# Optimization experiments

Hardware: AMD Instinct MI355X
Metric: run time of the kernel (lower is better)

The kernel has to match this reference:

```python
import jax, jax.numpy as jnp
import numpy as np

D = 256  # MCB sketch/output dimension


def count_sketch(x, h, s, d=D):
    # x: [B,H,W,C] channel-last; h: [C] int hash indices in [0,d); s: [C] +/-1 signs
    xs = x * s
    return jnp.zeros(x.shape[:-1] + (d,), x.dtype).at[..., h].add(xs)


def mcb(x, y, h1, s1, h2, s2, d=D):
    # Compact bilinear pooling per spatial location. x,y: [B,C,H,W] -> [B,d,H,W]
    xt = jnp.moveaxis(x, 1, -1)
    yt = jnp.moveaxis(y, 1, -1)
    fx = jnp.fft.rfft(count_sketch(xt, h1, s1, d), axis=-1)
    fy = jnp.fft.rfft(count_sketch(yt, h2, s2, d), axis=-1)
    out = jnp.fft.irfft(fx * fy, n=d, axis=-1)  # circular convolution of the two sketches
    return jnp.moveaxis(out, -1, 1)


def setup_inputs() -> dict:
    key = jax.random.key(0)
    ks = jax.random.split(key, 10)
    B, C, H, W, ATTR = 64, 256, 28, 28, 300
    entity_feature = jax.random.normal(ks[0], (B, C, H, W), jnp.float32)
    attr_one_hot = jax.random.uniform(ks[1], (B, ATTR), jnp.float32)
    W_emb = jax.random.normal(ks[2], (C, ATTR), jnp.float32) * 0.05
    b_emb = jax.random.normal(ks[3], (C,), jnp.float32) * 0.01
    h1 = jax.random.randint(ks[4], (C,), 0, D, jnp.int32)
    h2 = jax.random.randint(ks[5], (C,), 0, D, jnp.int32)
    s1 = jnp.where(jax.random.bernoulli(ks[6], 0.5, (C,)), 1.0, -1.0).astype(jnp.float32)
    s2 = jnp.where(jax.random.bernoulli(ks[7], 0.5, (C,)), 1.0, -1.0).astype(jnp.float32)
    conv1_w = jax.random.normal(ks[8], (32, C), jnp.float32) * 0.05
    conv2_w = jax.random.normal(ks[9], (1, 32), jnp.float32) * 0.05
    return {"entity_feature": entity_feature, "attr_one_hot": attr_one_hot,
            "W_emb": W_emb, "b_emb": b_emb, "h1": h1, "s1": s1, "h2": h2, "s2": s2,
            "conv1_w": conv1_w, "conv2_w": conv2_w}


def reference(entity_feature, attr_one_hot, W_emb, b_emb, h1, s1, h2, s2, conv1_w, conv2_w):
    # textual embedding: Linear(attr_num -> 256)
    emb = attr_one_hot @ W_emb.T + b_emb                      # [B,256]
    attr = jnp.broadcast_to(emb[:, :, None, None], entity_feature.shape)  # expand_as
    mcb_feat = mcb(attr, entity_feature, h1, s1, h2, s2)      # [B,256,H,W]
    hidden = jax.nn.relu(jnp.einsum('bchw,oc->bohw', mcb_feat, conv1_w))  # conv1x1 256->32
    attr_map = jax.nn.sigmoid(jnp.einsum('bchw,oc->bohw', hidden, conv2_w))  # conv1x1 32->1
    attr_feature = attr_map * entity_feature
    return attr_map, attr_feature
```

## Files before the change

### kernel.cpp

```cpp
#include <hip/hip_runtime.h>
#include <math.h>

#define BATCH 64
#define CC    256
#define ATTRN 300
#define DD    256
#define HW    784
#define HW4   196
#define O1    32
#define TF4   49


__global__ __launch_bounds__(512) void k2_fused(
    const float* __restrict__ attr_one_hot,
    const float* __restrict__ W_emb,
    const float* __restrict__ b_emb,
    const int*   __restrict__ h1,
    const float* __restrict__ s1,
    const float* __restrict__ conv1_w,
    float* __restrict__ corrT)
{
    const int b = blockIdx.x, og = blockIdx.y;
    const int tid = threadIdx.x;
    const int t = tid & 255, kh = tid >> 8;
    const int o0 = og * 8;

    __shared__ float s_attr[ATTRN];
    __shared__ float s_sx[DD];
    __shared__ float s_w1[8][DD];
    __shared__ float s_part[8][DD];

    if (kh == 0) {
        s_sx[t] = 0.f;
        if (t < 75) {
            float4 a = *(const float4*)(attr_one_hot + b * ATTRN + 4 * t);
            *(float4*)&s_attr[4 * t] = a;
        }
    } else {
#pragma unroll
        for (int j = 0; j < 8; ++j) s_w1[j][t] = conv1_w[(o0 + j) * CC + t];
    }
    __syncthreads();

    if (kh == 0) {
        float acc = b_emb[t];
        const float* wr = W_emb + (size_t)t * ATTRN;
#pragma unroll 5
        for (int v = 0; v < 75; ++v) {
            float4 w = *(const float4*)(wr + 4 * v);
            float4 a = *(const float4*)(&s_attr[4 * v]);
            acc += w.x * a.x + w.y * a.y + w.z * a.z + w.w * a.w;
        }
        atomicAdd(&s_sx[h1[t]], s1[t] * acc);
    }
    __syncthreads();

    float acc[8] = {0.f,0.f,0.f,0.f,0.f,0.f,0.f,0.f};
    const int kbase = kh << 7;
    for (int k4 = 0; k4 < 32; ++k4) {
        const int k = kbase + 4 * k4;
        float x0 = s_sx[(k     - t) & 255];
        float x1 = s_sx[(k + 1 - t) & 255];
        float x2 = s_sx[(k + 2 - t) & 255];
        float x3 = s_sx[(k + 3 - t) & 255];
#pragma unroll
        for (int oo = 0; oo < 8; ++oo) {
            float4 w = *(const float4*)&s_w1[oo][k];
            acc[oo] += w.x * x0 + w.y * x1 + w.z * x2 + w.w * x3;
        }
    }
    if (kh == 1) {
#pragma unroll
        for (int oo = 0; oo < 8; ++oo) s_part[oo][t] = acc[oo];
    }
    __syncthreads();
    if (kh == 0) {
        float4 r0, r1;
        r0.x = acc[0] + s_part[0][t]; r0.y = acc[1] + s_part[1][t];
        r0.z = acc[2] + s_part[2][t]; r0.w = acc[3] + s_part[3][t];
        r1.x = acc[4] + s_part[4][t]; r1.y = acc[5] + s_part[5][t];
        r1.z = acc[6] + s_part[6][t]; r1.w = acc[7] + s_part[7][t];
        float4* dst = (float4*)(corrT + ((size_t)b * DD + t) * O1 + o0);
        dst[0] = r0; dst[1] = r1;
    }
}

#define FMA4(A, S, E) { (A).x += (S)*(E).x; (A).y += (S)*(E).y; (A).z += (S)*(E).z; (A).w += (S)*(E).w; }

__global__ __launch_bounds__(1024, 4) void k3_main(
    const float* __restrict__ ent,
    const float* __restrict__ corrT,
    const int*   __restrict__ h2,
    const float* __restrict__ s2,
    const float* __restrict__ conv2_w,
    float* __restrict__ out_map,
    float* __restrict__ out_feat)
{
    const int b = blockIdx.x, tile = blockIdx.y;
    const int tid  = threadIdx.x;
    const int wv   = tid >> 6, lane = tid & 63;
    const int ci   = wv >> 2;
    const int oi   = wv & 3;

    union SMem {
        float  Pl[CC][36];
        float4 red[4][TF4][9];
    };
    __shared__ SMem sm;
    __shared__ float4 s_amap4[TF4];
    __shared__ float  s_c2[O1];

    {
        const int c = tid >> 2, qp = tid & 3;
        const int hc = h2[c];
        const float sc = s2[c];
        const float4* src = (const float4*)(corrT + ((size_t)b * DD + hc) * O1);
        float4 x0 = src[2 * qp], x1 = src[2 * qp + 1];
        x0.x *= sc; x0.y *= sc; x0.z *= sc; x0.w *= sc;
        x1.x *= sc; x1.y *= sc; x1.z *= sc; x1.w *= sc;
        *(float4*)&sm.Pl[c][8 * qp]     = x0;
        *(float4*)&sm.Pl[c][8 * qp + 4] = x1;
        if (tid < O1) s_c2[tid] = conv2_w[tid];
    }
    __syncthreads();

    const bool act = lane < TF4;
    const int f4i = tile * TF4 + (act ? lane : TF4 - 1);
    const float4* ent4 = (const float4*)ent;
    const int c0 = ci * 64;

    float4 acc[8];
#pragma unroll
    for (int o = 0; o < 8; ++o) acc[o] = make_float4(0.f, 0.f, 0.f, 0.f);

    const float4* eptr = ent4 + (size_t)(b * CC + c0) * HW4 + f4i;
#pragma unroll 4
    for (int cc = 0; cc < 64; ++cc) {
        const int c = c0 + cc;
        float4 e4 = eptr[(size_t)cc * HW4];
        float4 pa = *(const float4*)&sm.Pl[c][8 * oi];
        float4 pb = *(const float4*)&sm.Pl[c][8 * oi + 4];
        FMA4(acc[0], pa.x, e4); FMA4(acc[1], pa.y, e4);
        FMA4(acc[2], pa.z, e4); FMA4(acc[3], pa.w, e4);
        FMA4(acc[4], pb.x, e4); FMA4(acc[5], pb.y, e4);
        FMA4(acc[6], pb.z, e4); FMA4(acc[7], pb.w, e4);
    }

    float pre = 0.f;
#pragma unroll
    for (int g = 0; g < 4; ++g) {
        __syncthreads();
        if (oi == g && act) {
#pragma unroll
            for (int i = 0; i < 8; ++i) sm.red[ci][lane][i] = acc[i];
        }
        __syncthreads();
        if (tid < 4 * TF4) {
            const int fi = tid >> 2, j = tid & 3;
#pragma unroll
            for (int i = 0; i < 8; ++i) {
                float v = ((const float*)&sm.red[0][fi][i])[j]
                        + ((const float*)&sm.red[1][fi][i])[j]
                        + ((const float*)&sm.red[2][fi][i])[j]
                        + ((const float*)&sm.red[3][fi][i])[j];
                pre += s_c2[8 * g + i] * fmaxf(v, 0.f);
            }
        }
    }
    __syncthreads();
    if (tid < 4 * TF4) {
        const int fi = tid >> 2, j = tid & 3;
        float am = 1.f / (1.f + expf(-pre));
        ((float*)&s_amap4[fi])[j] = am;
        out_map[b * HW + tile * (4 * TF4) + tid] = am;
    }
    __syncthreads();

    const float4 am4 = s_amap4[act ? lane : 0];
    float4* of4 = (float4*)out_feat;
    const int cb = wv * 16;
#pragma unroll 4
    for (int cc = 0; cc < 16; ++cc) {
        const int c = cb + cc;
        if (act) {
            const size_t idx = (size_t)(b * CC + c) * HW4 + f4i;
            float4 e4 = ent4[idx];
            float4 r;
            r.x = am4.x * e4.x; r.y = am4.y * e4.y;
            r.z = am4.z * e4.z; r.w = am4.w * e4.w;
            of4[idx] = r;
        }
    }
}

extern "C" void kernel_launch(void* const* d_in, const int* in_sizes, int n_in,
                              void* d_out, int out_size, void* d_ws, size_t ws_size,
                              hipStream_t stream) {
    const float* ent   = (const float*)d_in[0];
    const float* attr  = (const float*)d_in[1];
    const float* W_emb = (const float*)d_in[2];
    const float* b_emb = (const float*)d_in[3];
    const int*   h1    = (const int*)d_in[4];
    const float* s1    = (const float*)d_in[5];
    const int*   h2    = (const int*)d_in[6];
    const float* s2    = (const float*)d_in[7];
    const float* c1w   = (const float*)d_in[8];
    const float* c2w   = (const float*)d_in[9];

    float* ws    = (float*)d_ws;
    float* corrT = ws + 16384;

    float* out      = (float*)d_out;
    float* out_map  = out;
    float* out_feat = out + BATCH * HW;

    hipLaunchKernelGGL(k2_fused, dim3(BATCH, 4), dim3(512), 0, stream,
                       attr, W_emb, b_emb, h1, s1, c1w, corrT);
    hipLaunchKernelGGL(k3_main, dim3(BATCH, 4), dim3(1024), 0, stream,
                       ent, corrT, h2, s2, c2w, out_map, out_feat);
}
```

Measured before the change: 156.9 us.

## Stage entity feature loads into LDS via async global_load_lds double buffering

The channel loop of k3_main now streams entity features through a double-buffered LDS staging area using global_load_lds, prefetching the next 8-channel chunk while computing on the current one. The aim is to hide global memory latency, where before each iteration issued a direct global load per channel. The cost is a larger dynamic LDS footprint (about 100KB), a barrier per chunk, and a launch bound relaxed to one block per CU. Idle lanes still load clamped addresses, and the reduction scratch now reuses the staging buffer.

After: 148.8 us. 1.05x faster.

```diff
diff --git a/kernel.cpp b/kernel.cpp
--- a/kernel.cpp
+++ b/kernel.cpp
@@ -87,7 +87,17 @@
 
 #define FMA4(A, S, E) { (A).x += (S)*(E).x; (A).y += (S)*(E).y; (A).z += (S)*(E).z; (A).w += (S)*(E).w; }
 
-__global__ __launch_bounds__(1024, 4) void k3_main(
+#define PL_OFF 0
+#define ST_OFF 9216
+
+__device__ __forceinline__ void gld_lds16(const float4* g, float* l) {
+    __builtin_amdgcn_global_load_lds(
+        (__attribute__((address_space(1))) void*)g,
+        (__attribute__((address_space(3))) void*)l,
+        16, 0, 0);
+}
+
+__global__ __launch_bounds__(1024, 1) void k3_main(
     const float* __restrict__ ent,
     const float* __restrict__ corrT,
     const int*   __restrict__ h2,
@@ -96,19 +106,29 @@
     float* __restrict__ out_map,
     float* __restrict__ out_feat)
 {
+    extern __shared__ float lds[];
     const int b = blockIdx.x, tile = blockIdx.y;
     const int tid  = threadIdx.x;
     const int wv   = tid >> 6, lane = tid & 63;
     const int ci   = wv >> 2;
     const int oi   = wv & 3;
 
-    union SMem {
-        float  Pl[CC][36];
-        float4 red[4][TF4][9];
-    };
-    __shared__ SMem sm;
     __shared__ float4 s_amap4[TF4];
     __shared__ float  s_c2[O1];
+
+    const bool act = lane < TF4;
+    const int lclamp = act ? lane : (TF4 - 1);
+    const int f4i = tile * TF4 + lclamp;
+    const float4* ent4 = (const float4*)ent;
+    const int c0 = ci * 64;
+    const float4* gbase = ent4 + (size_t)(b * CC + c0) * HW4 + tile * TF4 + lclamp;
+
+    {
+        const int rr0 = 2 * oi;
+        float* d0 = &lds[ST_OFF + ci * 4096 + 0 * 2048 + rr0 * 256];
+        gld_lds16(gbase + (size_t)(rr0)     * HW4, d0);
+        gld_lds16(gbase + (size_t)(rr0 + 1) * HW4, d0 + 256);
+    }
 
     {
         const int c = tid >> 2, qp = tid & 3;
@@ -118,51 +138,56 @@
         float4 x0 = src[2 * qp], x1 = src[2 * qp + 1];
         x0.x *= sc; x0.y *= sc; x0.z *= sc; x0.w *= sc;
         x1.x *= sc; x1.y *= sc; x1.z *= sc; x1.w *= sc;
-        *(float4*)&sm.Pl[c][8 * qp]     = x0;
-        *(float4*)&sm.Pl[c][8 * qp + 4] = x1;
+        *(float4*)&lds[PL_OFF + c * 36 + 8 * qp]     = x0;
+        *(float4*)&lds[PL_OFF + c * 36 + 8 * qp + 4] = x1;
         if (tid < O1) s_c2[tid] = conv2_w[tid];
     }
     __syncthreads();
 
-    const bool act = lane < TF4;
-    const int f4i = tile * TF4 + (act ? lane : TF4 - 1);
-    const float4* ent4 = (const float4*)ent;
-    const int c0 = ci * 64;
-
     float4 acc[8];
 #pragma unroll
     for (int o = 0; o < 8; ++o) acc[o] = make_float4(0.f, 0.f, 0.f, 0.f);
 
-    const float4* eptr = ent4 + (size_t)(b * CC + c0) * HW4 + f4i;
-#pragma unroll 4
-    for (int cc = 0; cc < 64; ++cc) {
-        const int c = c0 + cc;
-        float4 e4 = eptr[(size_t)cc * HW4];
-        float4 pa = *(const float4*)&sm.Pl[c][8 * oi];
-        float4 pb = *(const float4*)&sm.Pl[c][8 * oi + 4];
-        FMA4(acc[0], pa.x, e4); FMA4(acc[1], pa.y, e4);
-        FMA4(acc[2], pa.z, e4); FMA4(acc[3], pa.w, e4);
-        FMA4(acc[4], pb.x, e4); FMA4(acc[5], pb.y, e4);
-        FMA4(acc[6], pb.z, e4); FMA4(acc[7], pb.w, e4);
-    }
-
+    for (int k = 0; k < 8; ++k) {
+        if (k < 7) {
+            const int rr0 = 2 * oi;
+            float* d0 = &lds[ST_OFF + ci * 4096 + ((k + 1) & 1) * 2048 + rr0 * 256];
+            gld_lds16(gbase + (size_t)((k + 1) * 8 + rr0)     * HW4, d0);
+            gld_lds16(gbase + (size_t)((k + 1) * 8 + rr0 + 1) * HW4, d0 + 256);
+        }
+        const float* sb = &lds[ST_OFF + ci * 4096 + (k & 1) * 2048 + 4 * lane];
+#pragma unroll
+        for (int cc = 0; cc < 8; ++cc) {
+            const int c = c0 + k * 8 + cc;
+            float4 e4 = *(const float4*)(sb + cc * 256);
+            float4 pa = *(const float4*)&lds[PL_OFF + c * 36 + 8 * oi];
+            float4 pb = *(const float4*)&lds[PL_OFF + c * 36 + 8 * oi + 4];
+            FMA4(acc[0], pa.x, e4); FMA4(acc[1], pa.y, e4);
+            FMA4(acc[2], pa.z, e4); FMA4(acc[3], pa.w, e4);
+            FMA4(acc[4], pb.x, e4); FMA4(acc[5], pb.y, e4);
+            FMA4(acc[6], pb.z, e4); FMA4(acc[7], pb.w, e4);
+        }
+        __syncthreads();
+    }
+
+    float4* red = (float4*)&lds[ST_OFF];
     float pre = 0.f;
 #pragma unroll
     for (int g = 0; g < 4; ++g) {
         __syncthreads();
         if (oi == g && act) {
 #pragma unroll
-            for (int i = 0; i < 8; ++i) sm.red[ci][lane][i] = acc[i];
+            for (int i = 0; i < 8; ++i) red[(ci * TF4 + lane) * 9 + i] = acc[i];
         }
         __syncthreads();
         if (tid < 4 * TF4) {
             const int fi = tid >> 2, j = tid & 3;
 #pragma unroll
             for (int i = 0; i < 8; ++i) {
-                float v = ((const float*)&sm.red[0][fi][i])[j]
-                        + ((const float*)&sm.red[1][fi][i])[j]
-                        + ((const float*)&sm.red[2][fi][i])[j]
-                        + ((const float*)&sm.red[3][fi][i])[j];
+                float v = ((const float*)&red[(0 * TF4 + fi) * 9 + i])[j]
+                        + ((const float*)&red[(1 * TF4 + fi) * 9 + i])[j]
+                        + ((const float*)&red[(2 * TF4 + fi) * 9 + i])[j]
+                        + ((const float*)&red[(3 * TF4 + fi) * 9 + i])[j];
                 pre += s_c2[8 * g + i] * fmaxf(v, 0.f);
             }
         }
@@ -216,6 +241,7 @@
 
     hipLaunchKernelGGL(k2_fused, dim3(BATCH, 4), dim3(512), 0, stream,
                        attr, W_emb, b_emb, h1, s1, c1w, corrT);
-    hipLaunchKernelGGL(k3_main, dim3(BATCH, 4), dim3(1024), 0, stream,
+    hipLaunchKernelGGL(k3_main, dim3(BATCH, 4), dim3(1024),
+                       (9216 + 16384) * sizeof(float), stream,
                        ent, corrT, h2, s2, c2w, out_map, out_feat);
 }
```
